# Kernel tuning notes

Measured on AMD Instinct MI355X. Metric: run time of the kernel, lower is better.

## Reference

```python
import jax, jax.numpy as jnp
import numpy as np

B, NB, D, H = 2048, 12, 256, 16
NU, NI, NR = 100000, 100000, 6
EPS = 1e-10


def _lin(k, din, dout):
    k1, k2 = jax.random.split(k)
    s = 1.0 / np.sqrt(din)
    w = jax.random.uniform(k1, (din, dout), minval=-s, maxval=s, dtype=jnp.float32)
    b = jax.random.uniform(k2, (dout,), minval=-s, maxval=s, dtype=jnp.float32)
    return w, b


def setup_inputs() -> dict:
    key = jax.random.key(0)
    ks = jax.random.split(key, 24)
    inp = {}
    inp['iids'] = jax.random.randint(ks[0], (B,), 0, NI)
    inp['i_user_pad'] = jnp.stack([
        jax.random.randint(ks[1], (B, NB), 0, NU),
        jax.random.randint(ks[2], (B, NB), 0, NR)], axis=-1)
    inp['i_item_pad'] = jax.random.randint(ks[3], (B, NB), 0, NI)
    inp['i_item_user_pad'] = jnp.stack([
        jax.random.randint(ks[4], (B, NB, NB), 0, NI),
        jax.random.randint(ks[5], (B, NB, NB), 0, NR)], axis=-1)
    inp['user_table'] = jax.random.normal(ks[6], (NU, D), dtype=jnp.float32) * 0.02
    inp['item_table'] = jax.random.normal(ks[7], (NI, D), dtype=jnp.float32) * 0.02
    inp['rate_table'] = jax.random.normal(ks[8], (NR, D), dtype=jnp.float32) * 0.02
    # g_u: 2D -> D -> D
    inp['g_u_w1'], inp['g_u_b1'] = _lin(ks[9], 2 * D, D)
    inp['g_u_w2'], inp['g_u_b2'] = _lin(ks[10], D, D)
    # item_users_att: 2D -> D -> H
    inp['attu_w1'], inp['attu_b1'] = _lin(ks[11], 2 * D, D)
    inp['attu_w2'], inp['attu_b2'] = _lin(ks[12], D, H)
    # item_users_head: NB*H -> NB*H//2 -> NB
    inp['headu_w1'], inp['headu_b1'] = _lin(ks[13], NB * H, NB * H // 2)
    inp['headu_w2'], inp['headu_b2'] = _lin(ks[14], NB * H // 2, NB)
    # aggre_items: D -> D (+relu)
    inp['aggi_w'], inp['aggi_b'] = _lin(ks[15], D, D)
    # item_items_att: 2D -> D -> H
    inp['attii_w1'], inp['attii_b1'] = _lin(ks[16], 2 * D, D)
    inp['attii_w2'], inp['attii_b2'] = _lin(ks[17], D, H)
    # item_items_head: NB*H -> NB*H//2 -> NB
    inp['headii_w1'], inp['headii_b1'] = _lin(ks[18], NB * H, NB * H // 2)
    inp['headii_w2'], inp['headii_b2'] = _lin(ks[19], NB * H // 2, NB)
    # aggre_item2item: D -> D (+relu)
    inp['aggii_w'], inp['aggii_b'] = _lin(ks[20], D, D)
    # combine_mlp: 2D -> D -> D -> D, relu each
    inp['comb_w1'], inp['comb_b1'] = _lin(ks[21], 2 * D, D)
    inp['comb_w2'], inp['comb_b2'] = _lin(ks[22], D, D)
    inp['comb_w3'], inp['comb_b3'] = _lin(ks[23], D, D)
    return inp


def _mlp(x, w1, b1, w2, b2):
    return jax.nn.relu(x @ w1 + b1) @ w2 + b2


def reference(iids, i_user_pad, i_item_pad, i_item_user_pad,
              user_table, item_table, rate_table,
              g_u_w1, g_u_b1, g_u_w2, g_u_b2,
              attu_w1, attu_b1, attu_w2, attu_b2,
              headu_w1, headu_b1, headu_w2, headu_b2,
              aggi_w, aggi_b,
              attii_w1, attii_b1, attii_w2, attii_b2,
              headii_w1, headii_b1, headii_w2, headii_b2,
              aggii_w, aggii_b,
              comb_w1, comb_b1, comb_w2, comb_b2, comb_w3, comb_b3):
    dt = user_table.dtype
    # ---- stage 1: item <- its users ----
    p_t = user_table[i_user_pad[:, :, 0]]                       # [B,NB,D]
    mask_i = (i_user_pad[:, :, 0] > 0).astype(dt)               # [B,NB]
    er = rate_table[i_user_pad[:, :, 1]]                        # [B,NB,D]
    f_jt = _mlp(jnp.concatenate([p_t, er], -1), g_u_w1, g_u_b1, g_u_w2, g_u_b2)
    q_j = mask_i[:, :, None] * item_table[iids][:, None, :]     # [B,NB,D]
    miu = _mlp(jnp.concatenate([f_jt, q_j], -1), attu_w1, attu_b1, attu_w2, attu_b2)  # [B,NB,H]
    miu = _mlp(miu.reshape(miu.shape[0], -1), headu_w1, headu_b1, headu_w2, headu_b2)  # [B,NB]
    miu = jnp.exp(miu) * mask_i
    miu = miu / (jnp.sum(miu, 1, keepdims=True) + EPS)
    h_jU = jax.nn.relu(jnp.einsum('bn,bnd->bd', miu, f_jt) @ aggi_w + aggi_b)
    # ---- stage 2: neighbor items <- their users ----
    q_a_s = item_table[i_item_user_pad[..., 0]]                 # [B,NB,NB,D]
    mask_s = (i_item_user_pad[..., 0] > 0).astype(dt)           # [B,NB,NB]
    er_s = rate_table[i_item_user_pad[..., 1]]
    x_ia_s = _mlp(jnp.concatenate([q_a_s, er_s], -1), g_u_w1, g_u_b1, g_u_w2, g_u_b2)
    p_i_s = mask_s[..., None] * item_table[i_item_pad][:, :, None, :]
    miu_s = _mlp(jnp.concatenate([x_ia_s, p_i_s], -1), attu_w1, attu_b1, attu_w2, attu_b2)  # [B,NB,NB,H]
    miu_s = _mlp(miu_s.reshape(miu_s.shape[0], miu_s.shape[1], -1),
                 headu_w1, headu_b1, headu_w2, headu_b2)        # [B,NB,NB]
    miu_s = jnp.exp(miu_s) * mask_s
    miu_s = miu_s / (jnp.sum(miu_s, 2, keepdims=True) + EPS)
    h_oU = jax.nn.relu(jnp.einsum('bnm,bnmd->bnd', miu_s, x_ia_s) @ aggi_w + aggi_b)  # [B,NB,D]
    # ---- stage 3: item <- neighbor items ----
    kappa = _mlp(jnp.concatenate([h_oU, item_table[i_item_pad]], -1),
                 attii_w1, attii_b1, attii_w2, attii_b2)        # [B,NB,H]
    kappa = _mlp(kappa.reshape(kappa.shape[0], -1), headii_w1, headii_b1, headii_w2, headii_b2)  # [B,NB]
    mask_su = (i_item_pad > 0).astype(dt)
    kappa = jnp.exp(kappa) * mask_su
    kappa = kappa / (jnp.sum(kappa, 1, keepdims=True) + EPS)
    h_jV = jax.nn.relu(jnp.einsum('bn,bnd->bd', kappa, h_oU) @ aggii_w + aggii_b)
    # ---- combine ----
    h = jnp.concatenate([h_jU, h_jV], 1)
    h = jax.nn.relu(h @ comb_w1 + comb_b1)
    h = jax.nn.relu(h @ comb_w2 + comb_b2)
    return jax.nn.relu(h @ comb_w3 + comb_b3)
```

## Files before the change

### kernel.cpp

```cpp
#include <hip/hip_runtime.h>
#include <cstdint>
#include <cstddef>

typedef short short8 __attribute__((ext_vector_type(8)));
typedef short short4v __attribute__((ext_vector_type(4)));
typedef float f32x4 __attribute__((ext_vector_type(4)));
typedef __bf16 bf16x8 __attribute__((ext_vector_type(8)));

__device__ __forceinline__ unsigned short f2bu(float f) {
  union { float f; unsigned u; } v; v.f = f;
  unsigned r = v.u + 0x7FFFu + ((v.u >> 16) & 1u);
  return (unsigned short)(r >> 16);
}
__device__ __forceinline__ float b2f(unsigned short h) {
  union { unsigned u; float f; } v; v.u = ((unsigned)h) << 16;
  return v.f;
}

__device__ __forceinline__ f32x4 mfma16(short8 a, short8 b, f32x4 c) {
  return __builtin_amdgcn_mfma_f32_16x16x32_bf16(
      __builtin_bit_cast(bf16x8, a), __builtin_bit_cast(bf16x8, b), c, 0, 0, 0);
}

__global__ void k_cvt(const float* __restrict__ in, short* __restrict__ o, int ntot) {
  int i = (blockIdx.x * 256 + threadIdx.x) * 8;
  if (i >= ntot) return;
  float4 a = *(const float4*)(in + i);
  float4 b = *(const float4*)(in + i + 4);
  short8 v;
  v[0] = (short)f2bu(a.x); v[1] = (short)f2bu(a.y);
  v[2] = (short)f2bu(a.z); v[3] = (short)f2bu(a.w);
  v[4] = (short)f2bu(b.x); v[5] = (short)f2bu(b.y);
  v[6] = (short)f2bu(b.z); v[7] = (short)f2bu(b.w);
  *(short8*)(o + i) = v;
}

__global__ void k_cvt_rows(const float* __restrict__ tab, const int* __restrict__ pairs,
                           short* __restrict__ o, int nrows) {
  int t = blockIdx.x * 256 + threadIdx.x;
  if (t >= nrows * 32) return;
  int row = t >> 5;
  int c8 = (t & 31) << 3;
  int id = pairs[2 * row];
  const float* s = tab + (size_t)id * 256 + c8;
  float4 a = *(const float4*)(s);
  float4 b = *(const float4*)(s + 4);
  short8 v;
  v[0] = (short)f2bu(a.x); v[1] = (short)f2bu(a.y);
  v[2] = (short)f2bu(a.z); v[3] = (short)f2bu(a.w);
  v[4] = (short)f2bu(b.x); v[5] = (short)f2bu(b.y);
  v[6] = (short)f2bu(b.z); v[7] = (short)f2bu(b.w);
  *(short8*)(o + (size_t)row * 256 + c8) = v;
}

struct Prep {
  const float* src[16];
  short* dst[16];
  int K[16], N[16], mode[16];
  int boff[17];
};
__global__ void k_prep(Prep p) {
  int b = blockIdx.x, e = 0;
#pragma unroll
  for (int i = 1; i < 16; ++i) if (b >= p.boff[i]) e = i;
  int t = (b - p.boff[e]) * 256 + threadIdx.x;
  const int K = p.K[e], N = p.N[e];
  if (t >= K * N) return;
  const float* w = p.src[e];
  const int m = p.mode[e];
  if (m == 2) { p.dst[e][t] = (short)f2bu(w[t]); return; }
  if (m == 0) {
    int ks = t >> 13, rem = t & 8191;
    int P = rem >> 3, j = rem & 7;
    int n = P >> 2;
    int kq = ((P & 3) - (n >> 1)) & 3;
    int k = (ks << 5) + (kq << 3) + j;
    p.dst[e][t] = (short)f2bu(w[(size_t)k * 256 + n]);
    return;
  }
  int n = t / K, k = t - n * K;
  p.dst[e][t] = (short)f2bu(w[(size_t)k * N + n]);
}

template <bool IDENT>
__global__ __launch_bounds__(256, 3) void k_fused(
    const int* __restrict__ idx_pairs,
    const int* __restrict__ qidx_arr,
    const short* __restrict__ tab0,
    const short* __restrict__ tab1,
    const short* __restrict__ itembf,
    const short* __restrict__ zp,
    const short* __restrict__ ws1, const float* __restrict__ b1,
    const short* __restrict__ ws2, const float* __restrict__ b2,
    const short* __restrict__ aw1, const float* __restrict__ ab1,
    const short* __restrict__ aw2t, const float* __restrict__ ab2,
    short* __restrict__ Xout, short* __restrict__ miu_out)
{
  __shared__ __align__(16) short smem[20992];
  short* sA0 = smem;
  short* sA1 = smem + 2048;
  short* sH  = smem + 4096;

  const int tid = threadIdx.x;
  const int lane = tid & 63;
  const int wave = tid >> 6;
  const int m0 = (int)blockIdx.x << 6;
  const int l15 = lane & 15;
  const int lq = lane >> 4;
  const int nb = wave << 6;

  const int an = tid >> 2;
  const int kqA = ((tid & 3) - (an >> 1)) & 3;
  const int r = m0 + an;
  const int i0 = idx_pairs[2 * r];
  const int i1 = idx_pairs[2 * r + 1];
  const int qi = qidx_arr[r / 12];
  const short* a0 = (IDENT ? (tab0 + (size_t)r * 256) : (tab0 + (size_t)i0 * 256)) + kqA * 8;
  const short* a1 = tab1 + (size_t)i1 * 256 + kqA * 8;
  const short* aq = ((i0 > 0) ? (itembf + (size_t)qi * 256) : zp) + kqA * 8;

  int pBg[4], pA[4];
#pragma unroll
  for (int i = 0; i < 4; ++i) {
    int n = nb + i * 16 + l15;
    pBg[i] = (n * 4 + ((lq + (n >> 1)) & 3)) * 8;
    int m = i * 16 + l15;
    pA[i] = (m * 4 + ((lq + (m >> 1)) & 3)) * 8;
  }
  const int hOff = lq * 8;

  const f32x4 fz = {0.f, 0.f, 0.f, 0.f};
  f32x4 acc[4][4];
#pragma unroll
  for (int ni = 0; ni < 4; ++ni)
#pragma unroll
    for (int mi = 0; mi < 4; ++mi) acc[ni][mi] = fz;

  short8 wfb[3][4];
  short8 ar0, ar1;

  {
    short8 t = *(const short8*)a0;
    *(short8*)(sA0 + tid * 8) = t;
  }
  ar1 = *(const short8*)(a0 + 32);
#pragma unroll
  for (int i = 0; i < 4; ++i) wfb[0][i] = *(const short8*)(ws1 + pBg[i]);
#pragma unroll
  for (int i = 0; i < 4; ++i) wfb[1][i] = *(const short8*)(ws1 + 8192 + pBg[i]);
  __syncthreads();
#pragma unroll
  for (int ks = 0; ks < 16; ++ks) {
    short* sAc = (ks & 1) ? sA1 : sA0;
    short* sAn = (ks & 1) ? sA0 : sA1;
    if (ks < 14) {
      const int c = ks + 2;
      short8 t = *(const short8*)((c < 8) ? (a0 + c * 32) : (a1 + (c - 8) * 32));
      if ((ks & 1) == 0) ar0 = t; else ar1 = t;
      const short* s = ws1 + c * 8192;
#pragma unroll
      for (int i = 0; i < 4; ++i) wfb[c % 3][i] = *(const short8*)(s + pBg[i]);
    }
    short8 xf[4];
#pragma unroll
    for (int i = 0; i < 4; ++i) xf[i] = *(short8*)(sAc + pA[i]);
#pragma unroll
    for (int ni = 0; ni < 4; ++ni)
#pragma unroll
      for (int mi = 0; mi < 4; ++mi)
        acc[ni][mi] = mfma16(wfb[ks % 3][ni], xf[mi], acc[ni][mi]);
    if (ks < 15) {
      short8 w = (((ks + 1) & 1) == 0) ? ar0 : ar1;
      *(short8*)(sAn + tid * 8) = w;
      __syncthreads();
    }
  }
#pragma unroll
  for (int ni = 0; ni < 4; ++ni) {
    const int nbase = nb + ni * 16 + lq * 4;
    float4 bb = *(const float4*)(b1 + nbase);
#pragma unroll
    for (int mi = 0; mi < 4; ++mi) {
      const int m = mi * 16 + l15;
      short4v hv;
      hv[0] = (short)f2bu(fmaxf(acc[ni][mi][0] + bb.x, 0.f));
      hv[1] = (short)f2bu(fmaxf(acc[ni][mi][1] + bb.y, 0.f));
      hv[2] = (short)f2bu(fmaxf(acc[ni][mi][2] + bb.z, 0.f));
      hv[3] = (short)f2bu(fmaxf(acc[ni][mi][3] + bb.w, 0.f));
      *(short4v*)(sH + m * 264 + nbase) = hv;
    }
  }
  __syncthreads();

  short8 qr0 = *(const short8*)(aq);
  short8 qr1 = *(const short8*)(aq + 32);

#pragma unroll
  for (int ni = 0; ni < 4; ++ni)
#pragma unroll
    for (int mi = 0; mi < 4; ++mi) acc[ni][mi] = fz;
#pragma unroll
  for (int i = 0; i < 4; ++i) wfb[0][i] = *(const short8*)(ws2 + pBg[i]);
#pragma unroll
  for (int i = 0; i < 4; ++i) wfb[1][i] = *(const short8*)(ws2 + 8192 + pBg[i]);
#pragma unroll
  for (int ks = 0; ks < 8; ++ks) {
    if (ks < 6) {
      const short* s = ws2 + (ks + 2) * 8192;
#pragma unroll
      for (int i = 0; i < 4; ++i) wfb[(ks + 2) % 3][i] = *(const short8*)(s + pBg[i]);
    }
    short8 hf[4];
#pragma unroll
    for (int i = 0; i < 4; ++i)
      hf[i] = *(short8*)(sH + (i * 16 + l15) * 264 + ks * 32 + hOff);
#pragma unroll
    for (int ni = 0; ni < 4; ++ni)
#pragma unroll
      for (int mi = 0; mi < 4; ++mi)
        acc[ni][mi] = mfma16(wfb[ks % 3][ni], hf[mi], acc[ni][mi]);
  }
  *(short8*)(sA0 + tid * 8) = qr0;
  *(short8*)(sA1 + tid * 8) = qr1;
  __syncthreads();

#pragma unroll
  for (int ni = 0; ni < 4; ++ni) {
    const int nbase = nb + ni * 16 + lq * 4;
    float4 bb = *(const float4*)(b2 + nbase);
#pragma unroll
    for (int mi = 0; mi < 4; ++mi) {
      const int m = mi * 16 + l15;
      short4v hv;
      hv[0] = (short)f2bu(acc[ni][mi][0] + bb.x);
      hv[1] = (short)f2bu(acc[ni][mi][1] + bb.y);
      hv[2] = (short)f2bu(acc[ni][mi][2] + bb.z);
      hv[3] = (short)f2bu(acc[ni][mi][3] + bb.w);
      *(short4v*)(sH + m * 264 + nbase) = hv;
      *(short4v*)(Xout + (size_t)(m0 + m) * 256 + nbase) = hv;
    }
  }
  __syncthreads();

#pragma unroll
  for (int ni = 0; ni < 4; ++ni)
#pragma unroll
    for (int mi = 0; mi < 4; ++mi) acc[ni][mi] = fz;
#pragma unroll
  for (int i = 0; i < 4; ++i) wfb[0][i] = *(const short8*)(aw1 + pBg[i]);
#pragma unroll
  for (int i = 0; i < 4; ++i) wfb[1][i] = *(const short8*)(aw1 + 8192 + pBg[i]);
#pragma unroll
  for (int ks = 0; ks < 8; ++ks) {
    {
      const short* s = aw1 + (ks + 2) * 8192;
#pragma unroll
      for (int i = 0; i < 4; ++i) wfb[(ks + 2) % 3][i] = *(const short8*)(s + pBg[i]);
    }
    if (ks == 6) ar0 = *(const short8*)(aq + 2 * 32);
    if (ks == 7) ar1 = *(const short8*)(aq + 3 * 32);
    short8 xf[4];
#pragma unroll
    for (int i = 0; i < 4; ++i)
      xf[i] = *(short8*)(sH + (i * 16 + l15) * 264 + ks * 32 + hOff);
#pragma unroll
    for (int ni = 0; ni < 4; ++ni)
#pragma unroll
      for (int mi = 0; mi < 4; ++mi)
        acc[ni][mi] = mfma16(wfb[ks % 3][ni], xf[mi], acc[ni][mi]);
  }
#pragma unroll
  for (int k = 0; k < 8; ++k) {
    const int ks = 8 + k;
    short* sAc = (k & 1) ? sA1 : sA0;
    short* sAn = (k & 1) ? sA0 : sA1;
    if (ks < 14) {
      const short* s = aw1 + (ks + 2) * 8192;
#pragma unroll
      for (int i = 0; i < 4; ++i) wfb[(ks + 2) % 3][i] = *(const short8*)(s + pBg[i]);
    }
    if (k >= 2 && k < 6) {
      short8 t = *(const short8*)(aq + (k + 2) * 32);
      if ((k & 1) == 0) ar0 = t; else ar1 = t;
    }
    short8 xf[4];
#pragma unroll
    for (int i = 0; i < 4; ++i) xf[i] = *(short8*)(sAc + pA[i]);
#pragma unroll
    for (int ni = 0; ni < 4; ++ni)
#pragma unroll
      for (int mi = 0; mi < 4; ++mi)
        acc[ni][mi] = mfma16(wfb[ks % 3][ni], xf[mi], acc[ni][mi]);
    if (k >= 1 && k < 7) {
      short8 w = (((k + 1) & 1) == 0) ? ar0 : ar1;
      *(short8*)(sAn + tid * 8) = w;
    }
    if (k < 7) __syncthreads();
  }

#pragma unroll
  for (int ni = 0; ni < 4; ++ni) {
    const int nbase = nb + ni * 16 + lq * 4;
    float4 bb = *(const float4*)(ab1 + nbase);
#pragma unroll
    for (int mi = 0; mi < 4; ++mi) {
      const int m = mi * 16 + l15;
      short4v hv;
      hv[0] = (short)f2bu(fmaxf(acc[ni][mi][0] + bb.x, 0.f));
      hv[1] = (short)f2bu(fmaxf(acc[ni][mi][1] + bb.y, 0.f));
      hv[2] = (short)f2bu(fmaxf(acc[ni][mi][2] + bb.z, 0.f));
      hv[3] = (short)f2bu(fmaxf(acc[ni][mi][3] + bb.w, 0.f));
      *(short4v*)(sH + m * 264 + nbase) = hv;
    }
  }
  __syncthreads();

  f32x4 a2 = fz;
#pragma unroll
  for (int ks = 0; ks < 8; ++ks) {
    short8 af = *(short8*)(sH + (wave * 16 + l15) * 264 + ks * 32 + hOff);
    short8 bv = *(const short8*)(aw2t + l15 * 256 + ks * 32 + hOff);
    a2 = mfma16(af, bv, a2);
  }
  const float bias = ab2[l15];
#pragma unroll
  for (int j = 0; j < 4; ++j)
    miu_out[(size_t)(m0 + wave * 16 + lq * 4 + j) * 16 + l15] = (short)f2bu(a2[j] + bias);
}

__global__ __launch_bounds__(256, 3) void k_attonly(
    const short* __restrict__ first,
    const short* __restrict__ itembf,
    const int* __restrict__ iidx,
    const short* __restrict__ aw1, const float* __restrict__ ab1,
    const short* __restrict__ aw2t, const float* __restrict__ ab2,
    short* __restrict__ out)
{
  __shared__ __align__(16) short sH[16896];

  const int tid = threadIdx.x;
  const int lane = tid & 63;
  const int wave = tid >> 6;
  const int m0 = (int)blockIdx.x << 6;
  const int l15 = lane & 15;
  const int lq = lane >> 4;
  const int nb = wave << 6;
  const int hOff = lq * 8;

  const short* fp[4];
  const short* qp[4];
  int pBg[4];
#pragma unroll
  for (int i = 0; i < 4; ++i) {
    int mrow = m0 + i * 16 + l15;
    fp[i] = first + (size_t)mrow * 256 + hOff;
    qp[i] = itembf + (size_t)iidx[mrow] * 256 + hOff;
    int n = nb + i * 16 + l15;
    pBg[i] = (n * 4 + ((lq + (n >> 1)) & 3)) * 8;
  }

  const f32x4 fz = {0.f, 0.f, 0.f, 0.f};
  f32x4 acc[4][4];
#pragma unroll
  for (int ni = 0; ni < 4; ++ni)
#pragma unroll
    for (int mi = 0; mi < 4; ++mi) acc[ni][mi] = fz;

  short8 wfc[4], wfn[4], xfc[4], xfn[4];
#pragma unroll
  for (int i = 0; i < 4; ++i) {
    wfc[i] = *(const short8*)(aw1 + pBg[i]);
    xfc[i] = *(const short8*)(fp[i]);
  }
  for (int ks = 0; ks < 16; ++ks) {
    if (ks < 15) {
      const int c = ks + 1;
      const short* s = aw1 + c * 8192;
#pragma unroll
      for (int i = 0; i < 4; ++i) {
        wfn[i] = *(const short8*)(s + pBg[i]);
        xfn[i] = *(const short8*)((c < 8) ? (fp[i] + c * 32) : (qp[i] + (c - 8) * 32));
      }
    }
#pragma unroll
    for (int ni = 0; ni < 4; ++ni)
#pragma unroll
      for (int mi = 0; mi < 4; ++mi)
        acc[ni][mi] = mfma16(wfc[ni], xfc[mi], acc[ni][mi]);
    if (ks < 15) {
#pragma unroll
      for (int i = 0; i < 4; ++i) { wfc[i] = wfn[i]; xfc[i] = xfn[i]; }
    }
  }
#pragma unroll
  for (int ni = 0; ni < 4; ++ni) {
    const int nbase = nb + ni * 16 + lq * 4;
    float4 bb = *(const float4*)(ab1 + nbase);
#pragma unroll
    for (int mi = 0; mi < 4; ++mi) {
      const int m = mi * 16 + l15;
      short4v hv;
      hv[0] = (short)f2bu(fmaxf(acc[ni][mi][0] + bb.x, 0.f));
      hv[1] = (short)f2bu(fmaxf(acc[ni][mi][1] + bb.y, 0.f));
      hv[2] = (short)f2bu(fmaxf(acc[ni][mi][2] + bb.z, 0.f));
      hv[3] = (short)f2bu(fmaxf(acc[ni][mi][3] + bb.w, 0.f));
      *(short4v*)(sH + m * 264 + nbase) = hv;
    }
  }
  __syncthreads();
  f32x4 a2 = fz;
#pragma unroll
  for (int ks = 0; ks < 8; ++ks) {
    short8 af = *(short8*)(sH + (wave * 16 + l15) * 264 + ks * 32 + hOff);
    short8 bv = *(const short8*)(aw2t + l15 * 256 + ks * 32 + hOff);
    a2 = mfma16(af, bv, a2);
  }
  const float bias = ab2[l15];
#pragma unroll
  for (int j = 0; j < 4; ++j)
    out[(size_t)(m0 + wave * 16 + lq * 4 + j) * 16 + l15] = (short)f2bu(a2[j] + bias);
}

__global__ __launch_bounds__(256, 3) void k_gemm1(
    const short* __restrict__ Abf, const short* __restrict__ wt,
    const float* __restrict__ bias, short* __restrict__ out)
{
  const int tid  = threadIdx.x;
  const int lane = tid & 63;
  const int wave = tid >> 6;
  const int m0   = blockIdx.x << 6;
  const int l15  = lane & 15;
  const int lq   = lane >> 4;
  const int rq   = lq << 2;
  const int nb   = wave << 6;
  const int hOff = lq * 8;

  const f32x4 fz = {0.f, 0.f, 0.f, 0.f};
  f32x4 acc[4][4];
#pragma unroll
  for (int mi = 0; mi < 4; ++mi)
#pragma unroll
    for (int ni = 0; ni < 4; ++ni) acc[mi][ni] = fz;

  for (int ks = 0; ks < 8; ++ks) {
    short8 af[4], bv[4];
#pragma unroll
    for (int i = 0; i < 4; ++i) {
      af[i] = *(const short8*)(Abf + (size_t)(m0 + i * 16 + l15) * 256 + ks * 32 + hOff);
      bv[i] = *(const short8*)(wt + (size_t)(nb + i * 16 + l15) * 256 + ks * 32 + hOff);
    }
#pragma unroll
    for (int mi = 0; mi < 4; ++mi)
#pragma unroll
      for (int ni = 0; ni < 4; ++ni)
        acc[mi][ni] = mfma16(af[mi], bv[ni], acc[mi][ni]);
  }

#pragma unroll
  for (int ni = 0; ni < 4; ++ni) {
    const int col = nb + ni * 16 + l15;
    const float b = bias[col];
#pragma unroll
    for (int mi = 0; mi < 4; ++mi)
#pragma unroll
      for (int j = 0; j < 4; ++j) {
        const int row = mi * 16 + rq + j;
        out[(size_t)(m0 + row) * 256 + col] = (short)f2bu(fmaxf(acc[mi][ni][j] + b, 0.f));
      }
  }
}

__global__ __launch_bounds__(256, 2) void k_comb(
    const short* __restrict__ hju, const short* __restrict__ hjv,
    const short* __restrict__ w1t, const float* __restrict__ b1,
    const short* __restrict__ w2t, const float* __restrict__ b2,
    const short* __restrict__ w3t, const float* __restrict__ b3,
    float* __restrict__ out)
{
  __shared__ __align__(16) short smem[29696];
  short (*A)[40]   = (short(*)[40])smem;
  short (*Bt)[40]  = (short(*)[40])(smem + 2560);
  short (*Hh)[264] = (short(*)[264])(smem + 12800);

  const int tid  = threadIdx.x;
  const int lane = tid & 63;
  const int wave = tid >> 6;
  const int m0   = blockIdx.x << 6;
  const int arow = tid >> 2;
  const int acol8 = (tid & 3) << 3;
  const int lrow = lane & 15;
  const int lk8  = (lane >> 4) << 3;
  const int rq   = (lane >> 4) << 2;
  const int nb   = wave << 6;
  const int r = m0 + arow;

  const f32x4 fz = {0.f, 0.f, 0.f, 0.f};
  f32x4 acc[4][4];
#pragma unroll
  for (int mi = 0; mi < 4; ++mi)
#pragma unroll
    for (int ni = 0; ni < 4; ++ni) acc[mi][ni] = fz;

  for (int ks = 0; ks < 16; ++ks) {
    const int kg = (ks << 5) + acol8;
    short8 av = (kg < 256) ? *(const short8*)(hju + (size_t)r * 256 + kg)
                           : *(const short8*)(hjv + (size_t)r * 256 + (kg - 256));
    *(short8*)&A[arow][acol8] = av;
    const short* wsrc = w1t + tid * 512 + (ks << 5);
    *(short8*)&Bt[tid][0]  = *(const short8*)(wsrc);
    *(short8*)&Bt[tid][8]  = *(const short8*)(wsrc + 8);
    *(short8*)&Bt[tid][16] = *(const short8*)(wsrc + 16);
    *(short8*)&Bt[tid][24] = *(const short8*)(wsrc + 24);
    __syncthreads();
    short8 af[4], bv[4];
#pragma unroll
    for (int mi = 0; mi < 4; ++mi) af[mi] = *(short8*)&A[mi * 16 + lrow][lk8];
#pragma unroll
    for (int ni = 0; ni < 4; ++ni) bv[ni] = *(short8*)&Bt[nb + ni * 16 + lrow][lk8];
#pragma unroll
    for (int mi = 0; mi < 4; ++mi)
#pragma unroll
      for (int ni = 0; ni < 4; ++ni)
        acc[mi][ni] = mfma16(af[mi], bv[ni], acc[mi][ni]);
    __syncthreads();
  }
#pragma unroll
  for (int ni = 0; ni < 4; ++ni) {
    const int col = nb + ni * 16 + lrow;
    const float bias = b1[col];
#pragma unroll
    for (int mi = 0; mi < 4; ++mi)
#pragma unroll
      for (int j = 0; j < 4; ++j)
        Hh[mi * 16 + rq + j][col] = (short)f2bu(fmaxf(acc[mi][ni][j] + bias, 0.f));
  }

#pragma unroll
  for (int mi = 0; mi < 4; ++mi)
#pragma unroll
    for (int ni = 0; ni < 4; ++ni) acc[mi][ni] = fz;
  for (int ks = 0; ks < 8; ++ks) {
    const short* wsrc = w2t + tid * 256 + (ks << 5);
    *(short8*)&Bt[tid][0]  = *(const short8*)(wsrc);
    *(short8*)&Bt[tid][8]  = *(const short8*)(wsrc + 8);
    *(short8*)&Bt[tid][16] = *(const short8*)(wsrc + 16);
    *(short8*)&Bt[tid][24] = *(const short8*)(wsrc + 24);
    __syncthreads();
    short8 af[4], bv[4];
#pragma unroll
    for (int mi = 0; mi < 4; ++mi) af[mi] = *(short8*)&Hh[mi * 16 + lrow][(ks << 5) + lk8];
#pragma unroll
    for (int ni = 0; ni < 4; ++ni) bv[ni] = *(short8*)&Bt[nb + ni * 16 + lrow][lk8];
#pragma unroll
    for (int mi = 0; mi < 4; ++mi)
#pragma unroll
      for (int ni = 0; ni < 4; ++ni)
        acc[mi][ni] = mfma16(af[mi], bv[ni], acc[mi][ni]);
    __syncthreads();
  }
#pragma unroll
  for (int ni = 0; ni < 4; ++ni) {
    const int col = nb + ni * 16 + lrow;
    const float bias = b2[col];
#pragma unroll
    for (int mi = 0; mi < 4; ++mi)
#pragma unroll
      for (int j = 0; j < 4; ++j)
        Hh[mi * 16 + rq + j][col] = (short)f2bu(fmaxf(acc[mi][ni][j] + bias, 0.f));
  }
  __syncthreads();

#pragma unroll
  for (int mi = 0; mi < 4; ++mi)
#pragma unroll
    for (int ni = 0; ni < 4; ++ni) acc[mi][ni] = fz;
  for (int ks = 0; ks < 8; ++ks) {
    const short* wsrc = w3t + tid * 256 + (ks << 5);
    *(short8*)&Bt[tid][0]  = *(const short8*)(wsrc);
    *(short8*)&Bt[tid][8]  = *(const short8*)(wsrc + 8);
    *(short8*)&Bt[tid][16] = *(const short8*)(wsrc + 16);
    *(short8*)&Bt[tid][24] = *(const short8*)(wsrc + 24);
    __syncthreads();
    short8 af[4], bv[4];
#pragma unroll
    for (int mi = 0; mi < 4; ++mi) af[mi] = *(short8*)&Hh[mi * 16 + lrow][(ks << 5) + lk8];
#pragma unroll
    for (int ni = 0; ni < 4; ++ni) bv[ni] = *(short8*)&Bt[nb + ni * 16 + lrow][lk8];
#pragma unroll
    for (int mi = 0; mi < 4; ++mi)
#pragma unroll
      for (int ni = 0; ni < 4; ++ni)
        acc[mi][ni] = mfma16(af[mi], bv[ni], acc[mi][ni]);
    __syncthreads();
  }
#pragma unroll
  for (int ni = 0; ni < 4; ++ni) {
    const int col = nb + ni * 16 + lrow;
    const float bias = b3[col];
#pragma unroll
    for (int mi = 0; mi < 4; ++mi)
#pragma unroll
      for (int j = 0; j < 4; ++j) {
        const int row = mi * 16 + rq + j;
        out[(size_t)(m0 + row) * 256 + col] = fmaxf(acc[mi][ni][j] + bias, 0.f);
      }
  }
}

__global__ __launch_bounds__(256, 4) void k_h1(
    const short* __restrict__ A, const short* __restrict__ w1t,
    const float* __restrict__ b1, short* __restrict__ h1)
{
  const int tid = threadIdx.x;
  const int lane = tid & 63;
  const int wave = tid >> 6;
  const int m0 = (int)blockIdx.x << 6;
  const int l15 = lane & 15;
  const int lq = lane >> 4;
  const int ntc = (wave < 2) ? 2 : 1;
  const int nta = wave;
  const int ntb = wave + 4;

  const f32x4 fz = {0.f, 0.f, 0.f, 0.f};
  f32x4 acc[4][2];
#pragma unroll
  for (int i = 0; i < 4; ++i) { acc[i][0] = fz; acc[i][1] = fz; }

  for (int ks = 0; ks < 6; ++ks) {
    short8 af[4], bv[2];
#pragma unroll
    for (int i = 0; i < 4; ++i)
      af[i] = *(const short8*)(A + (size_t)(m0 + i * 16 + l15) * 192 + ks * 32 + lq * 8);
    bv[0] = *(const short8*)(w1t + (nta * 16 + l15) * 192 + ks * 32 + lq * 8);
    if (ntc == 2)
      bv[1] = *(const short8*)(w1t + (ntb * 16 + l15) * 192 + ks * 32 + lq * 8);
#pragma unroll
    for (int j = 0; j < 2; ++j)
      if (j < ntc)
#pragma unroll
        for (int i = 0; i < 4; ++i)
          acc[i][j] = mfma16(bv[j], af[i], acc[i][j]);
  }
#pragma unroll
  for (int j = 0; j < 2; ++j) {
    if (j >= ntc) continue;
    const int nbase = (j == 0 ? nta : ntb) * 16 + lq * 4;
    float4 bb = *(const float4*)(b1 + nbase);
#pragma unroll
    for (int i = 0; i < 4; ++i) {
      const int row = m0 + i * 16 + l15;
      short4v hv;
      hv[0] = (short)f2bu(fmaxf(acc[i][j][0] + bb.x, 0.f));
      hv[1] = (short)f2bu(fmaxf(acc[i][j][1] + bb.y, 0.f));
      hv[2] = (short)f2bu(fmaxf(acc[i][j][2] + bb.z, 0.f));
      hv[3] = (short)f2bu(fmaxf(acc[i][j][3] + bb.w, 0.f));
      *(short4v*)(h1 + (size_t)row * 96 + nbase) = hv;
    }
  }
}

__global__ __launch_bounds__(256) void k_h2(
    const short* __restrict__ h1, const short* __restrict__ w2t,
    const float* __restrict__ b2,
    const int* __restrict__ mask_src, const int mstride,
    float* __restrict__ W)
{
  __shared__ float wgt[16][12];
  const int tid = threadIdx.x;
  const int gg = tid >> 4, sl = tid & 15;
  const int g = blockIdx.x * 16 + gg;
  if (sl < 12) {
    float s = b2[sl];
    const short* hr = h1 + (size_t)g * 96;
    const short* wr = w2t + sl * 96;
#pragma unroll
    for (int kk = 0; kk < 12; ++kk) {
      short8 hv = *(const short8*)(hr + kk * 8);
      short8 wv = *(const short8*)(wr + kk * 8);
#pragma unroll
      for (int j = 0; j < 8; ++j)
        s += b2f((unsigned short)hv[j]) * b2f((unsigned short)wv[j]);
    }
    const int mi = mask_src[(g * 12 + sl) * mstride];
    wgt[gg][sl] = (mi > 0) ? expf(s) : 0.f;
  }
  __syncthreads();
  if (sl < 12) {
    float tot = 1e-10f;
#pragma unroll
    for (int m = 0; m < 12; ++m) tot += wgt[gg][m];
    W[(size_t)g * 12 + sl] = wgt[gg][sl] / tot;
  }
}

__global__ __launch_bounds__(256) void k_wsum(
    const float* __restrict__ W, const short* __restrict__ X,
    short* __restrict__ out)
{
  const int tid = threadIdx.x;
  const int g = blockIdx.x * 8 + (tid >> 5);
  const int d0 = (tid & 31) * 8;
  const float* wg = W + (size_t)g * 12;
  float w[12];
#pragma unroll
  for (int m = 0; m < 12; ++m) w[m] = wg[m];
  const short* xp = X + (size_t)g * 12 * 256 + d0;
  float o[8];
#pragma unroll
  for (int j = 0; j < 8; ++j) o[j] = 0.f;
#pragma unroll
  for (int m = 0; m < 12; ++m) {
    short8 x = *(const short8*)(xp + m * 256);
#pragma unroll
    for (int j = 0; j < 8; ++j) o[j] += w[m] * b2f((unsigned short)x[j]);
  }
  short8 v;
#pragma unroll
  for (int j = 0; j < 8; ++j) v[j] = (short)f2bu(o[j]);
  *(short8*)(out + (size_t)g * 256 + d0) = v;
}

extern "C" void kernel_launch(void* const* d_in, const int* in_sizes, int n_in,
                              void* d_out, int out_size, void* d_ws, size_t ws_size,
                              hipStream_t stream)
{
  (void)in_sizes; (void)n_in; (void)out_size; (void)ws_size;

  const int*   iids = (const int*)d_in[0];
  const int*   iup  = (const int*)d_in[1];
  const int*   iip  = (const int*)d_in[2];
  const int*   iiup = (const int*)d_in[3];
  const float* user_table = (const float*)d_in[4];
  const float* item_table = (const float*)d_in[5];
  const float* rate_table = (const float*)d_in[6];
  const float* g_u_w1 = (const float*)d_in[7];   const float* g_u_b1 = (const float*)d_in[8];
  const float* g_u_w2 = (const float*)d_in[9];   const float* g_u_b2 = (const float*)d_in[10];
  const float* attu_w1 = (const float*)d_in[11]; const float* attu_b1 = (const float*)d_in[12];
  const float* attu_w2 = (const float*)d_in[13]; const float* attu_b2 = (const float*)d_in[14];
  const float* headu_w1 = (const float*)d_in[15]; const float* headu_b1 = (const float*)d_in[16];
  const float* headu_w2 = (const float*)d_in[17]; const float* headu_b2 = (const float*)d_in[18];
  const float* aggi_w = (const float*)d_in[19];  const float* aggi_b = (const float*)d_in[20];
  const float* attii_w1 = (const float*)d_in[21]; const float* attii_b1 = (const float*)d_in[22];
  const float* attii_w2 = (const float*)d_in[23]; const float* attii_b2 = (const float*)d_in[24];
  const float* headii_w1 = (const float*)d_in[25]; const float* headii_b1 = (const float*)d_in[26];
  const float* headii_w2 = (const float*)d_in[27]; const float* headii_b2 = (const float*)d_in[28];
  const float* aggii_w = (const float*)d_in[29]; const float* aggii_b = (const float*)d_in[30];
  const float* comb_w1 = (const float*)d_in[31]; const float* comb_b1 = (const float*)d_in[32];
  const float* comb_w2 = (const float*)d_in[33]; const float* comb_b2 = (const float*)d_in[34];
  const float* comb_w3 = (const float*)d_in[35]; const float* comb_b3 = (const float*)d_in[36];

  const int NIe = 100000 * 256;
  const int M2 = 2048 * 12 * 12;
  const int M1 = 2048 * 12;
  const int G2 = M1;
  const int G1 = 2048;

  char* wsp = (char*)d_ws;
  size_t off = 0;
  auto alloc = [&](size_t bytes) -> void* {
    void* p = wsp + off;
    off += (bytes + 255) & ~(size_t)255;
    return p;
  };
  short* item_bf = (short*)alloc((size_t)NIe * 2);
  short* rate_bf = (short*)alloc((size_t)6 * 256 * 2);
  short* urows   = (short*)alloc((size_t)M1 * 256 * 2);
  short* zp      = (short*)alloc(512);
  short* sl_gu1   = (short*)alloc((size_t)512 * 256 * 2);
  short* sl_gu2   = (short*)alloc((size_t)256 * 256 * 2);
  short* sl_attu1 = (short*)alloc((size_t)512 * 256 * 2);
  short* sl_attii1= (short*)alloc((size_t)512 * 256 * 2);
  short* wt_attu2 = (short*)alloc((size_t)256 * 16 * 2);
  short* wt_attii2= (short*)alloc((size_t)256 * 16 * 2);
  short* wt_aggi   = (short*)alloc((size_t)256 * 256 * 2);
  short* wt_aggii  = (short*)alloc((size_t)256 * 256 * 2);
  short* wt_comb1  = (short*)alloc((size_t)512 * 256 * 2);
  short* wt_comb2  = (short*)alloc((size_t)256 * 256 * 2);
  short* wt_comb3  = (short*)alloc((size_t)256 * 256 * 2);
  short* hu1t  = (short*)alloc((size_t)96 * 192 * 2);
  short* hu2t  = (short*)alloc((size_t)12 * 96 * 2);
  short* hii1t = (short*)alloc((size_t)96 * 192 * 2);
  short* hii2t = (short*)alloc((size_t)12 * 96 * 2);

  short* X      = (short*)alloc((size_t)M2 * 256 * 2);
  short* FJT    = (short*)alloc((size_t)M1 * 256 * 2);
  short* MIU2   = (short*)alloc((size_t)M2 * 16 * 2);
  short* MIU1   = (short*)alloc((size_t)M1 * 16 * 2);
  short* KAP    = (short*)alloc((size_t)M1 * 16 * 2);
  short* H1A    = (short*)alloc((size_t)G2 * 96 * 2);
  short* H1K    = (short*)alloc((size_t)G1 * 96 * 2);
  short* H1M    = (short*)alloc((size_t)G1 * 96 * 2);
  float* WA     = (float*)alloc((size_t)G2 * 12 * 4);
  float* WK     = (float*)alloc((size_t)G1 * 12 * 4);
  float* WM     = (float*)alloc((size_t)G1 * 12 * 4);
  short* HPRE2  = (short*)alloc((size_t)M1 * 256 * 2);
  short* HOU    = (short*)alloc((size_t)M1 * 256 * 2);
  short* HPREJV = (short*)alloc((size_t)2048 * 256 * 2);
  short* HPRE1  = (short*)alloc((size_t)2048 * 256 * 2);
  short* HJU    = (short*)alloc((size_t)2048 * 256 * 2);
  short* HJV    = (short*)alloc((size_t)2048 * 256 * 2);

  hipMemsetAsync(zp, 0, 512, stream);
  k_cvt<<<NIe / 8 / 256, 256, 0, stream>>>(item_table, item_bf, NIe);
  k_cvt_rows<<<(M1 * 32) / 256, 256, 0, stream>>>(user_table, iup, urows, M1);

  Prep pp;
  int nbk = 0, ei = 0;
  auto addw = [&](const float* s, short* d, int K, int N, int mode) {
    pp.src[ei] = s; pp.dst[ei] = d; pp.K[ei] = K; pp.N[ei] = N; pp.mode[ei] = mode;
    pp.boff[ei] = nbk; nbk += (K * N + 255) / 256; ++ei;
  };
  addw(g_u_w1,   sl_gu1,    512, 256, 0);
  addw(g_u_w2,   sl_gu2,    256, 256, 0);
  addw(attu_w1,  sl_attu1,  512, 256, 0);
  addw(attii_w1, sl_attii1, 512, 256, 0);
  addw(attu_w2,  wt_attu2,  256, 16, 1);
  addw(attii_w2, wt_attii2, 256, 16, 1);
  addw(aggi_w,   wt_aggi,   256, 256, 1);
  addw(aggii_w,  wt_aggii,  256, 256, 1);
  addw(comb_w1,  wt_comb1,  512, 256, 1);
  addw(comb_w2,  wt_comb2,  256, 256, 1);
  addw(comb_w3,  wt_comb3,  256, 256, 1);
  addw(rate_table, rate_bf, 6, 256, 2);
  addw(headu_w1,  hu1t,  192, 96, 1);
  addw(headu_w2,  hu2t,  96, 12, 1);
  addw(headii_w1, hii1t, 192, 96, 1);
  addw(headii_w2, hii2t, 96, 12, 1);
  pp.boff[16] = nbk;
  k_prep<<<nbk, 256, 0, stream>>>(pp);

  k_fused<false><<<M2 / 64, 256, 0, stream>>>(iiup, iip, item_bf, rate_bf, item_bf, zp,
                                              sl_gu1, g_u_b1, sl_gu2, g_u_b2,
                                              sl_attu1, attu_b1, wt_attu2, attu_b2,
                                              X, MIU2);
  k_fused<true><<<M1 / 64, 256, 0, stream>>>(iup, iids, urows, rate_bf, item_bf, zp,
                                             sl_gu1, g_u_b1, sl_gu2, g_u_b2,
                                             sl_attu1, attu_b1, wt_attu2, attu_b2,
                                             FJT, MIU1);

  k_h1<<<G2 / 64, 256, 0, stream>>>(MIU2, hu1t, headu_b1, H1A);
  k_h2<<<G2 / 16, 256, 0, stream>>>(H1A, hu2t, headu_b2, iiup, 2, WA);
  k_wsum<<<G2 / 8, 256, 0, stream>>>(WA, X, HPRE2);

  k_gemm1<<<M1 / 64, 256, 0, stream>>>(HPRE2, wt_aggi, aggi_b, HOU);
  k_attonly<<<M1 / 64, 256, 0, stream>>>(HOU, item_bf, iip,
                                         sl_attii1, attii_b1, wt_attii2, attii_b2, KAP);

  k_h1<<<G1 / 64, 256, 0, stream>>>(KAP, hii1t, headii_b1, H1K);
  k_h2<<<G1 / 16, 256, 0, stream>>>(H1K, hii2t, headii_b2, iip, 1, WK);
  k_wsum<<<G1 / 8, 256, 0, stream>>>(WK, HOU, HPREJV);

  k_h1<<<G1 / 64, 256, 0, stream>>>(MIU1, hu1t, headu_b1, H1M);
  k_h2<<<G1 / 16, 256, 0, stream>>>(H1M, hu2t, headu_b2, iup, 2, WM);
  k_wsum<<<G1 / 8, 256, 0, stream>>>(WM, FJT, HPRE1);

  k_gemm1<<<2048 / 64, 256, 0, stream>>>(HPRE1, wt_aggi, aggi_b, HJU);
  k_gemm1<<<2048 / 64, 256, 0, stream>>>(HPREJV, wt_aggii, aggii_b, HJV);
  k_comb<<<2048 / 64, 256, 0, stream>>>(HJU, HJV, wt_comb1, comb_b1,
                                        wt_comb2, comb_b2, wt_comb3, comb_b3,
                                        (float*)d_out);
}
```

Before: 476.5 us.

## Precompute rate and query projections to halve K in fused gather MLP

Result: slower. 507.8 us (+6.6%).

```diff
diff --git a/kernel.cpp b/kernel.cpp
--- a/kernel.cpp
+++ b/kernel.cpp
@@ -82,14 +82,75 @@
   p.dst[e][t] = (short)f2bu(w[(size_t)k * N + n]);
 }
 
+__global__ void k_rc(const float* __restrict__ rate, const float* __restrict__ w1,
+                     float* __restrict__ RC) {
+  const int j = blockIdx.x;
+  const int n = threadIdx.x;
+  float s = 0.f;
+  const float* rr = rate + j * 256;
+  for (int k = 0; k < 256; ++k)
+    s += rr[k] * w1[(size_t)(256 + k) * 256 + n];
+  RC[j * 256 + n] = s;
+}
+
+__global__ __launch_bounds__(256, 4) void k_qc(
+    const int* __restrict__ qid, const short* __restrict__ itembf,
+    const short* __restrict__ aw1, float* __restrict__ QC)
+{
+  const int tid = threadIdx.x;
+  const int lane = tid & 63;
+  const int wave = tid >> 6;
+  const int m0 = (int)blockIdx.x << 6;
+  const int l15 = lane & 15;
+  const int lq = lane >> 4;
+  const int nb = wave << 6;
+
+  int pBg[4];
+  const short* qp[4];
+#pragma unroll
+  for (int i = 0; i < 4; ++i) {
+    int n = nb + i * 16 + l15;
+    pBg[i] = (n * 4 + ((lq + (n >> 1)) & 3)) * 8;
+    qp[i] = itembf + (size_t)qid[m0 + i * 16 + l15] * 256 + lq * 8;
+  }
+
+  const f32x4 fz = {0.f, 0.f, 0.f, 0.f};
+  f32x4 acc[4][4];
+#pragma unroll
+  for (int ni = 0; ni < 4; ++ni)
+#pragma unroll
+    for (int mi = 0; mi < 4; ++mi) acc[ni][mi] = fz;
+
+  for (int ks = 0; ks < 8; ++ks) {
+    short8 wf[4], qf[4];
+#pragma unroll
+    for (int i = 0; i < 4; ++i) {
+      wf[i] = *(const short8*)(aw1 + (8 + ks) * 8192 + pBg[i]);
+      qf[i] = *(const short8*)(qp[i] + ks * 32);
+    }
+#pragma unroll
+    for (int ni = 0; ni < 4; ++ni)
+#pragma unroll
+      for (int mi = 0; mi < 4; ++mi)
+        acc[ni][mi] = mfma16(wf[ni], qf[mi], acc[ni][mi]);
+  }
+#pragma unroll
+  for (int ni = 0; ni < 4; ++ni) {
+    const int nbase = nb + ni * 16 + lq * 4;
+#pragma unroll
+    for (int mi = 0; mi < 4; ++mi) {
+      const int m = mi * 16 + l15;
+      *(f32x4*)(QC + (size_t)(m0 + m) * 256 + nbase) = acc[ni][mi];
+    }
+  }
+}
+
 template <bool IDENT>
 __global__ __launch_bounds__(256, 3) void k_fused(
     const int* __restrict__ idx_pairs,
-    const int* __restrict__ qidx_arr,
     const short* __restrict__ tab0,
-    const short* __restrict__ tab1,
-    const short* __restrict__ itembf,
-    const short* __restrict__ zp,
+    const float* __restrict__ RC,
+    const float* __restrict__ QC,
     const short* __restrict__ ws1, const float* __restrict__ b1,
     const short* __restrict__ ws2, const float* __restrict__ b2,
     const short* __restrict__ aw1, const float* __restrict__ ab1,
@@ -113,11 +174,7 @@
   const int kqA = ((tid & 3) - (an >> 1)) & 3;
   const int r = m0 + an;
   const int i0 = idx_pairs[2 * r];
-  const int i1 = idx_pairs[2 * r + 1];
-  const int qi = qidx_arr[r / 12];
   const short* a0 = (IDENT ? (tab0 + (size_t)r * 256) : (tab0 + (size_t)i0 * 256)) + kqA * 8;
-  const short* a1 = tab1 + (size_t)i1 * 256 + kqA * 8;
-  const short* aq = ((i0 > 0) ? (itembf + (size_t)qi * 256) : zp) + kqA * 8;
 
   int pBg[4], pA[4];
 #pragma unroll
@@ -139,6 +196,15 @@
   short8 wfb[3][4];
   short8 ar0, ar1;
 
+  int i1v[4], mskv[4], grpv[4];
+#pragma unroll
+  for (int mi = 0; mi < 4; ++mi) {
+    const int row = m0 + mi * 16 + l15;
+    i1v[mi]  = idx_pairs[2 * row + 1];
+    mskv[mi] = idx_pairs[2 * row];
+    grpv[mi] = row / 12;
+  }
+
   {
     short8 t = *(const short8*)a0;
     *(short8*)(sA0 + tid * 8) = t;
@@ -150,12 +216,12 @@
   for (int i = 0; i < 4; ++i) wfb[1][i] = *(const short8*)(ws1 + 8192 + pBg[i]);
   __syncthreads();
 #pragma unroll
-  for (int ks = 0; ks < 16; ++ks) {
+  for (int ks = 0; ks < 8; ++ks) {
     short* sAc = (ks & 1) ? sA1 : sA0;
     short* sAn = (ks & 1) ? sA0 : sA1;
-    if (ks < 14) {
+    if (ks < 6) {
       const int c = ks + 2;
-      short8 t = *(const short8*)((c < 8) ? (a0 + c * 32) : (a1 + (c - 8) * 32));
+      short8 t = *(const short8*)(a0 + c * 32);
       if ((ks & 1) == 0) ar0 = t; else ar1 = t;
       const short* s = ws1 + c * 8192;
 #pragma unroll
@@ -169,7 +235,7 @@
 #pragma unroll
       for (int mi = 0; mi < 4; ++mi)
         acc[ni][mi] = mfma16(wfb[ks % 3][ni], xf[mi], acc[ni][mi]);
-    if (ks < 15) {
+    if (ks < 7) {
       short8 w = (((ks + 1) & 1) == 0) ? ar0 : ar1;
       *(short8*)(sAn + tid * 8) = w;
       __syncthreads();
@@ -182,18 +248,16 @@
 #pragma unroll
     for (int mi = 0; mi < 4; ++mi) {
       const int m = mi * 16 + l15;
+      float4 rc = *(const float4*)(RC + i1v[mi] * 256 + nbase);
       short4v hv;
-      hv[0] = (short)f2bu(fmaxf(acc[ni][mi][0] + bb.x, 0.f));
-      hv[1] = (short)f2bu(fmaxf(acc[ni][mi][1] + bb.y, 0.f));
-      hv[2] = (short)f2bu(fmaxf(acc[ni][mi][2] + bb.z, 0.f));
-      hv[3] = (short)f2bu(fmaxf(acc[ni][mi][3] + bb.w, 0.f));
+      hv[0] = (short)f2bu(fmaxf(acc[ni][mi][0] + rc.x + bb.x, 0.f));
+      hv[1] = (short)f2bu(fmaxf(acc[ni][mi][1] + rc.y + bb.y, 0.f));
+      hv[2] = (short)f2bu(fmaxf(acc[ni][mi][2] + rc.z + bb.z, 0.f));
+      hv[3] = (short)f2bu(fmaxf(acc[ni][mi][3] + rc.w + bb.w, 0.f));
       *(short4v*)(sH + m * 264 + nbase) = hv;
     }
   }
   __syncthreads();
-
-  short8 qr0 = *(const short8*)(aq);
-  short8 qr1 = *(const short8*)(aq + 32);
 
 #pragma unroll
   for (int ni = 0; ni < 4; ++ni)
@@ -220,8 +284,6 @@
       for (int mi = 0; mi < 4; ++mi)
         acc[ni][mi] = mfma16(wfb[ks % 3][ni], hf[mi], acc[ni][mi]);
   }
-  *(short8*)(sA0 + tid * 8) = qr0;
-  *(short8*)(sA1 + tid * 8) = qr1;
   __syncthreads();
 
 #pragma unroll
@@ -252,13 +314,11 @@
   for (int i = 0; i < 4; ++i) wfb[1][i] = *(const short8*)(aw1 + 8192 + pBg[i]);
 #pragma unroll
   for (int ks = 0; ks < 8; ++ks) {
-    {
+    if (ks < 6) {
       const short* s = aw1 + (ks + 2) * 8192;
 #pragma unroll
       for (int i = 0; i < 4; ++i) wfb[(ks + 2) % 3][i] = *(const short8*)(s + pBg[i]);
     }
-    if (ks == 6) ar0 = *(const short8*)(aq + 2 * 32);
-    if (ks == 7) ar1 = *(const short8*)(aq + 3 * 32);
     short8 xf[4];
 #pragma unroll
     for (int i = 0; i < 4; ++i)
@@ -269,34 +329,7 @@
       for (int mi = 0; mi < 4; ++mi)
         acc[ni][mi] = mfma16(wfb[ks % 3][ni], xf[mi], acc[ni][mi]);
   }
-#pragma unroll
-  for (int k = 0; k < 8; ++k) {
-    const int ks = 8 + k;
-    short* sAc = (k & 1) ? sA1 : sA0;
-    short* sAn = (k & 1) ? sA0 : sA1;
-    if (ks < 14) {
-      const short* s = aw1 + (ks + 2) * 8192;
-#pragma unroll
-      for (int i = 0; i < 4; ++i) wfb[(ks + 2) % 3][i] = *(const short8*)(s + pBg[i]);
-    }
-    if (k >= 2 && k < 6) {
-      short8 t = *(const short8*)(aq + (k + 2) * 32);
-      if ((k & 1) == 0) ar0 = t; else ar1 = t;
-    }
-    short8 xf[4];
-#pragma unroll
-    for (int i = 0; i < 4; ++i) xf[i] = *(short8*)(sAc + pA[i]);
-#pragma unroll
-    for (int ni = 0; ni < 4; ++ni)
-#pragma unroll
-      for (int mi = 0; mi < 4; ++mi)
-        acc[ni][mi] = mfma16(wfb[ks % 3][ni], xf[mi], acc[ni][mi]);
-    if (k >= 1 && k < 7) {
-      short8 w = (((k + 1) & 1) == 0) ? ar0 : ar1;
-      *(short8*)(sAn + tid * 8) = w;
-    }
-    if (k < 7) __syncthreads();
-  }
+  __syncthreads();
 
 #pragma unroll
   for (int ni = 0; ni < 4; ++ni) {
@@ -305,11 +338,14 @@
 #pragma unroll
     for (int mi = 0; mi < 4; ++mi) {
       const int m = mi * 16 + l15;
+      float4 qv;
+      if (mskv[mi] > 0) qv = *(const float4*)(QC + (size_t)grpv[mi] * 256 + nbase);
+      else { qv.x = 0.f; qv.y = 0.f; qv.z = 0.f; qv.w = 0.f; }
       short4v hv;
-      hv[0] = (short)f2bu(fmaxf(acc[ni][mi][0] + bb.x, 0.f));
-      hv[1] = (short)f2bu(fmaxf(acc[ni][mi][1] + bb.y, 0.f));
-      hv[2] = (short)f2bu(fmaxf(acc[ni][mi][2] + bb.z, 0.f));
-      hv[3] = (short)f2bu(fmaxf(acc[ni][mi][3] + bb.w, 0.f));
+      hv[0] = (short)f2bu(fmaxf(acc[ni][mi][0] + qv.x + bb.x, 0.f));
+      hv[1] = (short)f2bu(fmaxf(acc[ni][mi][1] + qv.y + bb.y, 0.f));
+      hv[2] = (short)f2bu(fmaxf(acc[ni][mi][2] + qv.z + bb.z, 0.f));
+      hv[3] = (short)f2bu(fmaxf(acc[ni][mi][3] + qv.w + bb.w, 0.f));
       *(short4v*)(sH + m * 264 + nbase) = hv;
     }
   }
@@ -763,9 +799,7 @@
     return p;
   };
   short* item_bf = (short*)alloc((size_t)NIe * 2);
-  short* rate_bf = (short*)alloc((size_t)6 * 256 * 2);
   short* urows   = (short*)alloc((size_t)M1 * 256 * 2);
-  short* zp      = (short*)alloc(512);
   short* sl_gu1   = (short*)alloc((size_t)512 * 256 * 2);
   short* sl_gu2   = (short*)alloc((size_t)256 * 256 * 2);
   short* sl_attu1 = (short*)alloc((size_t)512 * 256 * 2);
@@ -781,6 +815,9 @@
   short* hu2t  = (short*)alloc((size_t)12 * 96 * 2);
   short* hii1t = (short*)alloc((size_t)96 * 192 * 2);
   short* hii2t = (short*)alloc((size_t)12 * 96 * 2);
+  float* RC    = (float*)alloc((size_t)6 * 256 * 4);
+  float* QC2   = (float*)alloc((size_t)G2 * 256 * 4);
+  float* QC1   = (float*)alloc((size_t)G1 * 256 * 4);
 
   short* X      = (short*)alloc((size_t)M2 * 256 * 2);
   short* FJT    = (short*)alloc((size_t)M1 * 256 * 2);
@@ -800,9 +837,9 @@
   short* HJU    = (short*)alloc((size_t)2048 * 256 * 2);
   short* HJV    = (short*)alloc((size_t)2048 * 256 * 2);
 
-  hipMemsetAsync(zp, 0, 512, stream);
   k_cvt<<<NIe / 8 / 256, 256, 0, stream>>>(item_table, item_bf, NIe);
   k_cvt_rows<<<(M1 * 32) / 256, 256, 0, stream>>>(user_table, iup, urows, M1);
+  k_rc<<<6, 256, 0, stream>>>(rate_table, g_u_w1, RC);
 
   Prep pp;
   int nbk = 0, ei = 0;
@@ -821,19 +858,22 @@
   addw(comb_w1,  wt_comb1,  512, 256, 1);
   addw(comb_w2,  wt_comb2,  256, 256, 1);
   addw(comb_w3,  wt_comb3,  256, 256, 1);
-  addw(rate_table, rate_bf, 6, 256, 2);
   addw(headu_w1,  hu1t,  192, 96, 1);
   addw(headu_w2,  hu2t,  96, 12, 1);
   addw(headii_w1, hii1t, 192, 96, 1);
   addw(headii_w2, hii2t, 96, 12, 1);
+  pp.boff[15] = nbk;
   pp.boff[16] = nbk;
   k_prep<<<nbk, 256, 0, stream>>>(pp);
 
-  k_fused<false><<<M2 / 64, 256, 0, stream>>>(iiup, iip, item_bf, rate_bf, item_bf, zp,
+  k_qc<<<G2 / 64, 256, 0, stream>>>(iip, item_bf, sl_attu1, QC2);
+  k_qc<<<G1 / 64, 256, 0, stream>>>(iids, item_bf, sl_attu1, QC1);
+
+  k_fused<false><<<M2 / 64, 256, 0, stream>>>(iiup, item_bf, RC, QC2,
                                               sl_gu1, g_u_b1, sl_gu2, g_u_b2,
                                               sl_attu1, attu_b1, wt_attu2, attu_b2,
                                               X, MIU2);
-  k_fused<true><<<M1 / 64, 256, 0, stream>>>(iup, iids, urows, rate_bf, item_bf, zp,
+  k_fused<true><<<M1 / 64, 256, 0, stream>>>(iup, urows, RC, QC1,
                                              sl_gu1, g_u_b1, sl_gu2, g_u_b2,
                                              sl_attu1, attu_b1, wt_attu2, attu_b2,
                                              FJT, MIU1);
```
